# Kernel optimization log

Measured on AMD Instinct MI355X. Metric: run time of the kernel, lower is better.

The kernel has to match this reference:

```python
import jax, jax.numpy as jnp
import numpy as np

B, S, D = 8, 2048, 1024
N = 256          # state_dim
H = 512          # selector_hidden
E = 8            # num_experts


def murmurhash3_finalizer(token_ids):
    # Torch code works in int64 but masks to 32 bits after each multiply and
    # values stay non-negative, so it is exactly uint32 wrapping arithmetic.
    x = token_ids.astype(jnp.uint32)
    x = x ^ (x >> 16)
    x = x * jnp.uint32(2246822507)
    x = x ^ (x >> 13)
    x = x * jnp.uint32(3266489909)
    x = x ^ (x >> 16)
    return x


def setup_inputs() -> dict:
    key = jax.random.key(0)
    ks = jax.random.split(key, 7)
    scale = 0.02
    return {
        "x": jax.random.normal(ks[0], (B, S, D), dtype=jnp.float32),
        "token_ids": jax.random.randint(ks[1], (B, S), 0, 50257, dtype=jnp.int32),
        "Win": jax.random.normal(ks[2], (E, N, D), dtype=jnp.float32) * scale,      # in_proj.weight per expert
        "Wsin": jax.random.normal(ks[3], (E, H, D), dtype=jnp.float32) * scale,     # selector_in.weight
        "Wsout": jax.random.normal(ks[4], (E, 4 * N, H), dtype=jnp.float32) * scale,  # selector_out.weight
        "Wout": jax.random.normal(ks[5], (E, D, N), dtype=jnp.float32) * scale,     # out_proj.weight
        "dparam": jnp.ones((E, N), dtype=jnp.float32),                              # per-expert d
    }


def _forward(x, Win, Wsin, Wsout, Wout, dparam, token_ids):
    b, s, d = x.shape
    e_num, n, _ = Win.shape
    routes = (murmurhash3_finalizer(token_ids) % jnp.uint32(e_num)).astype(jnp.int32)  # (B,S)

    # Per-token expert projections, selected by hash route (masked accumulation
    # over the small fixed expert count; honors per-token routing).
    u = jnp.zeros((b, s, n), x.dtype)
    a = jnp.zeros((b, s, n), x.dtype)
    bg = jnp.zeros((b, s, n), x.dtype)
    c = jnp.zeros((b, s, n), x.dtype)
    dg = jnp.zeros((b, s, n), x.dtype)
    for e in range(e_num):
        m = (routes == e)[..., None]
        u = jnp.where(m, jnp.einsum('bsd,nd->bsn', x, Win[e]), u)
        sh = jax.nn.silu(jnp.einsum('bsd,hd->bsh', x, Wsin[e]))
        sel = jnp.einsum('bsh,oh->bso', sh, Wsout[e])       # (B,S,4N)
        ar, br, cr, dr = jnp.split(sel, 4, axis=-1)
        a = jnp.where(m, jax.nn.sigmoid(ar), a)
        bg = jnp.where(m, jnp.tanh(br), bg)
        c = jnp.where(m, jnp.tanh(cr), c)
        dg = jnp.where(m, jax.nn.sigmoid(dr), dg)

    dvec = dparam[routes]              # (B,S,N) expert d param per token
    skip = dvec * dg * u               # residual term, state-independent

    bidx = jnp.arange(b)

    def step(states, inp):
        # states: (B,E,N) per-expert hidden state per batch row
        route_t, u_t, a_t, b_t, c_t, skip_t = inp
        h_prev = states[bidx, route_t]                 # (B,N)
        h = a_t * h_prev + b_t * u_t
        states = states.at[bidx, route_t].set(h)       # only routed expert updates
        y = c_t * h + skip_t
        return states, y

    xs = (routes.swapaxes(0, 1), u.swapaxes(0, 1), a.swapaxes(0, 1),
          bg.swapaxes(0, 1), c.swapaxes(0, 1), skip.swapaxes(0, 1))
    states0 = jnp.zeros((b, e_num, n), x.dtype)
    _, ys = jax.lax.scan(step, states0, xs)            # ys: (S,B,N)
    y = ys.swapaxes(0, 1)                              # (B,S,N)

    out = jnp.zeros((b, s, d), x.dtype)
    for e in range(e_num):
        m = (routes == e)[..., None]
        out = jnp.where(m, jnp.einsum('bsn,dn->bsd', y, Wout[e]), out)
    return out


def reference(x, token_ids, Win, Wsin, Wsout, Wout, dparam):
    return _forward(x, Win, Wsin, Wsout, Wout, dparam, token_ids)
```

## Files before the change

kernel.cpp:

```cpp
#include <hip/hip_runtime.h>


#define TOKS 16384
#define RPAD 16512
#define DD   1024
#define NN   256
#define HH   512
#define MAXTILES  136
#define MAXCHUNKS 1088
#define CHUNK 16

typedef short short8 __attribute__((ext_vector_type(8)));
typedef float floatx4 __attribute__((ext_vector_type(4)));
typedef _Float16 half_t;

#define AS_GLOBAL __attribute__((address_space(1)))
#define AS_LDS    __attribute__((address_space(3)))

__device__ __forceinline__ void gl_lds16(const void* g, void* l) {
    __builtin_amdgcn_global_load_lds((const AS_GLOBAL void*)g, (AS_LDS void*)l, 16, 0, 0);
}

__device__ __forceinline__ unsigned short f2bf(float f) {
    union { float f; unsigned u; } c; c.f = f;
    unsigned r = c.u + 0x7FFF + ((c.u >> 16) & 1);
    return (unsigned short)(r >> 16);
}
__device__ __forceinline__ int route_of(int token) {
    unsigned x = (unsigned)token;
    x ^= x >> 16; x *= 2246822507u; x ^= x >> 13; x *= 3266489909u; x ^= x >> 16;
    return (int)(x & 7u);
}
__device__ __forceinline__ float sigm(float v) { return 1.0f / (1.0f + __expf(-v)); }
__device__ __forceinline__ float ftanh(float v) {
    float e = __expf(2.0f * v);
    return 1.0f - 2.0f / (e + 1.0f);
}

__global__ void k_route(const int* __restrict__ tok, int* __restrict__ cnt) {
    int b = blockIdx.x, tid = threadIdx.x;
    __shared__ int lc[256 * 8];
    #pragma unroll
    for (int e = 0; e < 8; e++) lc[tid * 8 + e] = 0;
    #pragma unroll
    for (int i = 0; i < 8; i++) {
        int e = route_of(tok[b * 2048 + tid * 8 + i]);
        lc[tid * 8 + e]++;
    }
    __syncthreads();
    if (tid < 8) {
        int s = 0;
        for (int t = 0; t < 256; t++) s += lc[t * 8 + tid];
        cnt[b * 8 + tid] = s;
    }
}

__global__ void k_offsets(const int* __restrict__ cnt, int* __restrict__ grpoff,
                          int* __restrict__ tileE, int* __restrict__ tileS,
                          int* __restrict__ tileR,
                          int* __restrict__ cGrp, int* __restrict__ cStart,
                          int* __restrict__ cLen, int* __restrict__ gBase,
                          int* __restrict__ meta) {
    __shared__ int sc[64], ce[8], eoff[9], etile[9], gb[65], go[64];
    int tid = threadIdx.x;
    if (tid < 64) sc[tid] = cnt[tid];
    __syncthreads();
    if (tid < 8) { int s = 0; for (int b = 0; b < 8; b++) s += sc[b * 8 + tid]; ce[tid] = s; }
    __syncthreads();
    if (tid == 0) {
        eoff[0] = 0; etile[0] = 0;
        for (int e = 0; e < 8; e++) {
            eoff[e + 1] = eoff[e] + ce[e];
            etile[e + 1] = etile[e] + (ce[e] + 127) / 128;
        }
        meta[0] = etile[8];
        gb[0] = 0;
        for (int g = 0; g < 64; g++) gb[g + 1] = gb[g] + (sc[g] + CHUNK - 1) / CHUNK;
        meta[1] = gb[64];
    }
    __syncthreads();
    if (tid < 64) {
        int b = tid >> 3, e = tid & 7;
        int run = eoff[e];
        for (int b2 = 0; b2 < b; b2++) run += sc[b2 * 8 + e];
        go[tid] = run;
        grpoff[tid] = run;
    }
    __syncthreads();
    if (tid < 8) {
        int e = tid, st = eoff[e], c = ce[e], t0 = etile[e];
        for (int i = 0, k = 0; i < c; i += 128, k++) {
            tileE[t0 + k] = e; tileS[t0 + k] = st + i;
            tileR[t0 + k] = (c - i < 128) ? (c - i) : 128;
        }
    }
    if (tid < 64) {
        int g = tid, n = sc[g], base = gb[g], s0 = go[g];
        gBase[g] = base;
        for (int i = 0, c = 0; i < n; i += CHUNK, c++) {
            cGrp[base + c] = g;
            cStart[base + c] = s0 + i;
            cLen[base + c] = (n - i < CHUNK) ? (n - i) : CHUNK;
        }
    }
}

__global__ void k_scatter(const int* __restrict__ tok, const int* __restrict__ grpoff,
                          int* __restrict__ perm) {
    int b = blockIdx.x, tid = threadIdx.x;
    __shared__ int lh[8 * 256];
    int r[8];
    int myc[8] = {0,0,0,0,0,0,0,0};
    #pragma unroll
    for (int i = 0; i < 8; i++) {
        int e = route_of(tok[b * 2048 + tid * 8 + i]);
        r[i] = e; myc[e]++;
    }
    #pragma unroll
    for (int e = 0; e < 8; e++) lh[e * 256 + tid] = myc[e];
    __syncthreads();
    for (int e = 0; e < 8; e++) {
        for (int off = 1; off < 256; off <<= 1) {
            int add = (tid >= off) ? lh[e * 256 + tid - off] : 0;
            __syncthreads();
            lh[e * 256 + tid] += add;
            __syncthreads();
        }
    }
    int basep[8];
    #pragma unroll
    for (int e = 0; e < 8; e++) basep[e] = grpoff[b * 8 + e] + lh[e * 256 + tid] - myc[e];
    #pragma unroll
    for (int i = 0; i < 8; i++) {
        int e = r[i];
        perm[basep[e]++] = b * 2048 + tid * 8 + i;
    }
}

__global__ void k_cvtw(const float* __restrict__ Win, const float* __restrict__ Wsin,
                       const float* __restrict__ Wsout, const float* __restrict__ Wout,
                       unsigned short* __restrict__ W12, unsigned short* __restrict__ Wso,
                       unsigned short* __restrict__ Wo) {
    const int C12 = 8 * 768 * 1024 / 4, CSO = 8 * 1024 * 512 / 4, CWO = 8 * 1024 * 256 / 4;
    int c = blockIdx.x * 256 + threadIdx.x;
    float4 v; unsigned short* dst;
    if (c < C12) {
        int d = c * 4;
        int e = d / (768 * 1024);
        int rem = d - e * (768 * 1024);
        int r = rem >> 10, k = rem & 1023;
        const float* src = (r < 256) ? (Win + (((size_t)e * 256 + r) << 10) + k)
                                     : (Wsin + (((size_t)e * 512 + (r - 256)) << 10) + k);
        v = *(const float4*)src;
        dst = W12 + d;
    } else if (c < C12 + CSO) {
        int d = (c - C12) * 4;
        v = *(const float4*)(Wsout + d);
        dst = Wso + d;
    } else if (c < C12 + CSO + CWO) {
        int d = (c - C12 - CSO) * 4;
        v = *(const float4*)(Wout + d);
        dst = Wo + d;
    } else return;
    ushort4 o;
    o.x = f2bf(v.x); o.y = f2bf(v.y); o.z = f2bf(v.z); o.w = f2bf(v.w);
    *(ushort4*)dst = o;
}

__global__ void k_gather(const float* __restrict__ x, const int* __restrict__ perm,
                         unsigned short* __restrict__ Xs, unsigned short* __restrict__ SHb,
                         unsigned short* __restrict__ Yb) {
    int r = blockIdx.x, t = threadIdx.x;
    if (r < TOKS) {
        int tok = perm[r];
        float4 v = *(const float4*)(x + (size_t)tok * 1024 + t * 4);
        ushort4 o;
        o.x = f2bf(v.x); o.y = f2bf(v.y); o.z = f2bf(v.z); o.w = f2bf(v.w);
        *(ushort4*)(Xs + (size_t)r * 1024 + t * 4) = o;
    } else {
        ushort4 z = {0, 0, 0, 0};
        *(ushort4*)(Xs + (size_t)r * 1024 + t * 4) = z;
        if (t < 128) *(ushort4*)(SHb + (size_t)r * 512 + t * 4) = z;
        if (t < 64)  *(ushort4*)(Yb + (size_t)r * 256 + t * 4) = z;
    }
}

template<int MODE, int KD>
__global__ __launch_bounds__(256, 3)
void k_mfma(const unsigned short* __restrict__ A, const unsigned short* __restrict__ Bw,
            const int* __restrict__ perm, const float* __restrict__ dparam,
            half_t* __restrict__ Ub, unsigned short* __restrict__ SHb,
            half_t* __restrict__ Aa, half_t* __restrict__ Wg,
            half_t* __restrict__ Cc, half_t* __restrict__ Sk,
            float* __restrict__ out,
            const int* __restrict__ tileE, const int* __restrict__ tileS,
            const int* __restrict__ tileR, const int* __restrict__ meta) {
    int mt = blockIdx.x;
    if (mt >= meta[0]) return;
    const int e = tileE[mt], pos0 = tileS[mt], rows = tileR[mt];
    const int col0 = blockIdx.y * 128;
    const int tid = threadIdx.x;
    const int w = tid >> 6, lane = tid & 63, quad = lane >> 4, l15 = lane & 15;
    const int wm = w & 1, wn = w >> 1;
    constexpr int NOUT = (MODE == 0) ? 768 : 1024;

    __shared__ unsigned short As[2 * 128 * 32];
    __shared__ unsigned short Bs[2 * 128 * 32];

    const int r0 = tid >> 2, c8 = (tid & 3) * 8;
    const unsigned short* ga = A + (size_t)(pos0 + r0) * KD + c8;
    const unsigned short* gb = Bw + ((size_t)e * NOUT + col0 + r0) * KD + c8;

    floatx4 acc[4][4] = {};

    int aoff[4], boff[4];
    #pragma unroll
    for (int i = 0; i < 4; i++) aoff[i] = (wm * 64 + i * 16 + l15) * 32 + quad * 8;
    #pragma unroll
    for (int j = 0; j < 4; j++) boff[j] = (wn * 64 + j * 16 + l15) * 32 + quad * 8;

    for (int k0 = 0; k0 < KD; k0 += 64) {
        __syncthreads();
        gl_lds16(ga + k0,                          As + w * 512);
        gl_lds16(ga + (size_t)64 * KD + k0,        As + 2048 + w * 512);
        gl_lds16(ga + k0 + 32,                     As + 4096 + w * 512);
        gl_lds16(ga + (size_t)64 * KD + k0 + 32,   As + 6144 + w * 512);
        gl_lds16(gb + k0,                          Bs + w * 512);
        gl_lds16(gb + (size_t)64 * KD + k0,        Bs + 2048 + w * 512);
        gl_lds16(gb + k0 + 32,                     Bs + 4096 + w * 512);
        gl_lds16(gb + (size_t)64 * KD + k0 + 32,   Bs + 6144 + w * 512);
        __syncthreads();
        #pragma unroll
        for (int kb = 0; kb < 2; kb++) {
            short8 af[4], bf[4];
            #pragma unroll
            for (int i = 0; i < 4; i++) af[i] = *(const short8*)(As + kb * 4096 + aoff[i]);
            #pragma unroll
            for (int j = 0; j < 4; j++) bf[j] = *(const short8*)(Bs + kb * 4096 + boff[j]);
            #pragma unroll
            for (int i = 0; i < 4; i++)
                #pragma unroll
                for (int j = 0; j < 4; j++)
                    acc[i][j] = __builtin_amdgcn_mfma_f32_16x16x32_bf16(af[i], bf[j], acc[i][j], 0, 0, 0);
        }
    }

    #pragma unroll
    for (int i = 0; i < 4; i++) {
        #pragma unroll
        for (int r = 0; r < 4; r++) {
            int m = wm * 64 + i * 16 + quad * 4 + r;
            if (m >= rows) continue;
            size_t row = (size_t)(pos0 + m);
            if (MODE == 0) {
                if (col0 < 256) {
                    #pragma unroll
                    for (int j = 0; j < 4; j++) {
                        int n = col0 + wn * 64 + j * 16 + l15;
                        Ub[row * 256 + n] = (half_t)acc[i][j][r];
                    }
                } else {
                    #pragma unroll
                    for (int j = 0; j < 4; j++) {
                        int n = col0 - 256 + wn * 64 + j * 16 + l15;
                        float v = acc[i][j][r];
                        SHb[row * 512 + n] = f2bf(v * sigm(v));
                    }
                }
            } else if (MODE == 1) {
                int region = col0 >> 8;
                #pragma unroll
                for (int j = 0; j < 4; j++) {
                    int n0 = (col0 & 255) + wn * 64 + j * 16 + l15;
                    size_t idx = row * 256 + (size_t)n0;
                    float v = acc[i][j][r];
                    if (region == 0) {
                        Aa[idx] = (half_t)sigm(v);
                    } else if (region == 1) {
                        Wg[idx] = (half_t)(ftanh(v) * (float)Ub[idx]);
                    } else if (region == 2) {
                        Cc[idx] = (half_t)ftanh(v);
                    } else {
                        Sk[idx] = (half_t)(dparam[e * 256 + n0] * sigm(v) * (float)Ub[idx]);
                    }
                }
            } else {
                int tok = perm[row];
                #pragma unroll
                for (int j = 0; j < 4; j++) {
                    int n = col0 + wn * 64 + j * 16 + l15;
                    out[(size_t)tok * 1024 + n] = acc[i][j][r];
                }
            }
        }
    }
}

__global__ void k_scanA(const half_t* __restrict__ Aa, const half_t* __restrict__ Wg,
                        const int* __restrict__ cStart, const int* __restrict__ cLen,
                        const int* __restrict__ meta,
                        float* __restrict__ SA, float* __restrict__ SQ) {
    int id = blockIdx.x;
    if (id >= meta[1]) return;
    int t = threadIdx.x;
    int s0 = cStart[id], L = cLen[id];
    size_t idx = (size_t)s0 * 256 + t;
    float p = 1.0f, q = 0.0f;
    for (int i = 0; i < L; i++) {
        float a = (float)Aa[idx], ww = (float)Wg[idx];
        q = a * q + ww;
        p *= a;
        idx += 256;
    }
    SA[(size_t)id * 256 + t] = p;
    SQ[(size_t)id * 256 + t] = q;
}

__global__ void k_scanB(const float* __restrict__ SA, const float* __restrict__ SQ,
                        const int* __restrict__ gBase, const int* __restrict__ cnt,
                        float* __restrict__ Hin) {
    int g = blockIdx.x, t = threadIdx.x;
    int base = gBase[g], nch = (cnt[g] + CHUNK - 1) / CHUNK;
    float h = 0.0f;
    for (int c = 0; c < nch; c++) {
        size_t k = (size_t)(base + c) * 256 + t;
        Hin[k] = h;
        h = SA[k] * h + SQ[k];
    }
}

__global__ void k_scanC(const half_t* __restrict__ Aa, const half_t* __restrict__ Wg,
                        const half_t* __restrict__ Cc, const half_t* __restrict__ Sk,
                        const int* __restrict__ cStart, const int* __restrict__ cLen,
                        const int* __restrict__ meta, const float* __restrict__ Hin,
                        unsigned short* __restrict__ Yb) {
    int id = blockIdx.x;
    if (id >= meta[1]) return;
    int t = threadIdx.x;
    int s0 = cStart[id], L = cLen[id];
    float h = Hin[(size_t)id * 256 + t];
    size_t idx = (size_t)s0 * 256 + t;
    for (int i = 0; i < L; i++) {
        float a = (float)Aa[idx], ww = (float)Wg[idx];
        float c = (float)Cc[idx], sk = (float)Sk[idx];
        h = a * h + ww;
        Yb[idx] = f2bf(c * h + sk);
        idx += 256;
    }
}

extern "C" void kernel_launch(void* const* d_in, const int* in_sizes, int n_in,
                              void* d_out, int out_size, void* d_ws, size_t ws_size,
                              hipStream_t stream) {
    const float* xin   = (const float*)d_in[0];
    const int*   tok   = (const int*)d_in[1];
    const float* Win   = (const float*)d_in[2];
    const float* Wsin  = (const float*)d_in[3];
    const float* Wsout = (const float*)d_in[4];
    const float* Wout  = (const float*)d_in[5];
    const float* dpar  = (const float*)d_in[6];
    float* out = (float*)d_out;

    size_t off = 0;
    char* base = (char*)d_ws;
    auto alloc = [&](size_t bytes) -> void* {
        void* p = base + off;
        off += (bytes + 255) & ~(size_t)255;
        return p;
    };
    half_t*         Ub  = (half_t*)alloc((size_t)RPAD * NN * 2);
    unsigned short* SHb = (unsigned short*)alloc((size_t)RPAD * HH * 2);
    unsigned short* Xs  = (unsigned short*)alloc((size_t)RPAD * DD * 2);
    unsigned short* Yb  = (unsigned short*)alloc((size_t)RPAD * NN * 2);
    half_t* Aa = (half_t*)alloc((size_t)TOKS * NN * 2);
    half_t* Wg = (half_t*)alloc((size_t)TOKS * NN * 2);
    half_t* Cc = (half_t*)alloc((size_t)TOKS * NN * 2);
    half_t* Sk = (half_t*)alloc((size_t)TOKS * NN * 2);
    unsigned short* W12 = (unsigned short*)alloc((size_t)8 * 768 * 1024 * 2);
    unsigned short* Wso = (unsigned short*)alloc((size_t)8 * 1024 * 512 * 2);
    unsigned short* Wo  = (unsigned short*)alloc((size_t)8 * 1024 * 256 * 2);
    float* SA  = (float*)alloc((size_t)MAXCHUNKS * 256 * 4);
    float* SQ  = (float*)alloc((size_t)MAXCHUNKS * 256 * 4);
    float* Hin = (float*)alloc((size_t)MAXCHUNKS * 256 * 4);
    int* perm   = (int*)alloc(TOKS * 4);
    int* cnt    = (int*)alloc(64 * 4);
    int* grpoff = (int*)alloc(64 * 4);
    int* tileE  = (int*)alloc(MAXTILES * 4);
    int* tileS  = (int*)alloc(MAXTILES * 4);
    int* tileR  = (int*)alloc(MAXTILES * 4);
    int* cGrp   = (int*)alloc(MAXCHUNKS * 4);
    int* cStart = (int*)alloc(MAXCHUNKS * 4);
    int* cLen   = (int*)alloc(MAXCHUNKS * 4);
    int* gBase  = (int*)alloc(64 * 4);
    int* meta   = (int*)alloc(16 * 4);

    k_route<<<8, 256, 0, stream>>>(tok, cnt);
    k_offsets<<<1, 256, 0, stream>>>(cnt, grpoff, tileE, tileS, tileR,
                                     cGrp, cStart, cLen, gBase, meta);
    k_scatter<<<8, 256, 0, stream>>>(tok, grpoff, perm);
    k_cvtw<<<12288, 256, 0, stream>>>(Win, Wsin, Wsout, Wout, W12, Wso, Wo);
    k_gather<<<RPAD, 256, 0, stream>>>(xin, perm, Xs, SHb, Yb);

    k_mfma<0, 1024><<<dim3(MAXTILES, 6), 256, 0, stream>>>(Xs, W12, perm, dpar,
        Ub, SHb, Aa, Wg, Cc, Sk, out, tileE, tileS, tileR, meta);
    k_mfma<1, 512><<<dim3(MAXTILES, 8), 256, 0, stream>>>(SHb, Wso, perm, dpar,
        Ub, SHb, Aa, Wg, Cc, Sk, out, tileE, tileS, tileR, meta);

    k_scanA<<<MAXCHUNKS, 256, 0, stream>>>(Aa, Wg, cStart, cLen, meta, SA, SQ);
    k_scanB<<<64, 256, 0, stream>>>(SA, SQ, gBase, cnt, Hin);
    k_scanC<<<MAXCHUNKS, 256, 0, stream>>>(Aa, Wg, Cc, Sk, cStart, cLen, meta, Hin, Yb);

    k_mfma<2, 256><<<dim3(MAXTILES, 8), 256, 0, stream>>>(Yb, Wo, perm, dpar,
        Ub, SHb, Aa, Wg, Cc, Sk, out, tileE, tileS, tileR, meta);
}
```

Before: 350.0 us.

## Double-buffer LDS tiles with async prefetch and XOR-swizzle to avoid bank conflicts

The MFMA GEMM main loop now ping-pongs between two LDS buffers of K=32 each, issuing global-to-LDS loads for the next slice before computing the current one, and uses explicit vmcnt waits and barriers. This overlaps memory latency with MFMA work instead of serializing load, sync and compute. It also XOR-swizzles the 8-element column chunk in both the store and the fragment read addresses to reduce LDS bank conflicts. In exchange each step covers half the previous K depth, so there are more barriers per tile, and correctness now depends on the hand-placed waitcnt counts.

```diff
diff --git a/kernel.cpp b/kernel.cpp
--- a/kernel.cpp
+++ b/kernel.cpp
@@ -203,47 +203,60 @@
     const int w = tid >> 6, lane = tid & 63, quad = lane >> 4, l15 = lane & 15;
     const int wm = w & 1, wn = w >> 1;
     constexpr int NOUT = (MODE == 0) ? 768 : 1024;
-
-    __shared__ unsigned short As[2 * 128 * 32];
-    __shared__ unsigned short Bs[2 * 128 * 32];
-
-    const int r0 = tid >> 2, c8 = (tid & 3) * 8;
-    const unsigned short* ga = A + (size_t)(pos0 + r0) * KD + c8;
-    const unsigned short* gb = Bw + ((size_t)e * NOUT + col0 + r0) * KD + c8;
+    constexpr int NK = KD / 32;
+
+    __shared__ unsigned short As[2][128 * 32];
+    __shared__ unsigned short Bs[2][128 * 32];
+
+    const int r0 = tid >> 2;
+    const int c8s = ((tid & 3) ^ ((tid >> 3) & 3)) * 8;
+    const unsigned short* ga = A + (size_t)(pos0 + r0) * KD + c8s;
+    const unsigned short* gb = Bw + ((size_t)e * NOUT + col0 + r0) * KD + c8s;
 
     floatx4 acc[4][4] = {};
 
+    const int sq = (quad ^ ((l15 >> 1) & 3)) * 8;
     int aoff[4], boff[4];
     #pragma unroll
-    for (int i = 0; i < 4; i++) aoff[i] = (wm * 64 + i * 16 + l15) * 32 + quad * 8;
-    #pragma unroll
-    for (int j = 0; j < 4; j++) boff[j] = (wn * 64 + j * 16 + l15) * 32 + quad * 8;
-
-    for (int k0 = 0; k0 < KD; k0 += 64) {
-        __syncthreads();
-        gl_lds16(ga + k0,                          As + w * 512);
-        gl_lds16(ga + (size_t)64 * KD + k0,        As + 2048 + w * 512);
-        gl_lds16(ga + k0 + 32,                     As + 4096 + w * 512);
-        gl_lds16(ga + (size_t)64 * KD + k0 + 32,   As + 6144 + w * 512);
-        gl_lds16(gb + k0,                          Bs + w * 512);
-        gl_lds16(gb + (size_t)64 * KD + k0,        Bs + 2048 + w * 512);
-        gl_lds16(gb + k0 + 32,                     Bs + 4096 + w * 512);
-        gl_lds16(gb + (size_t)64 * KD + k0 + 32,   Bs + 6144 + w * 512);
-        __syncthreads();
+    for (int i = 0; i < 4; i++) aoff[i] = (wm * 64 + i * 16 + l15) * 32 + sq;
+    #pragma unroll
+    for (int j = 0; j < 4; j++) boff[j] = (wn * 64 + j * 16 + l15) * 32 + sq;
+
+    #define STAGE(buf, k0) do { \
+        gl_lds16(ga + (k0),                    As[buf] + w * 512); \
+        gl_lds16(ga + (size_t)64 * KD + (k0),  As[buf] + 2048 + w * 512); \
+        gl_lds16(gb + (k0),                    Bs[buf] + w * 512); \
+        gl_lds16(gb + (size_t)64 * KD + (k0),  Bs[buf] + 2048 + w * 512); \
+    } while (0)
+
+    STAGE(0, 0);
+    for (int kt = 0; kt < NK; kt++) {
+        const int cur = kt & 1;
+        if (kt + 1 < NK) {
+            STAGE(cur ^ 1, (kt + 1) * 32);
+            asm volatile("s_waitcnt vmcnt(4)" ::: "memory");
+        } else {
+            asm volatile("s_waitcnt vmcnt(0)" ::: "memory");
+        }
+        __builtin_amdgcn_s_barrier();
+        asm volatile("" ::: "memory");
+        short8 af[4], bf[4];
         #pragma unroll
-        for (int kb = 0; kb < 2; kb++) {
-            short8 af[4], bf[4];
+        for (int i = 0; i < 4; i++) af[i] = *(const short8*)(As[cur] + aoff[i]);
+        #pragma unroll
+        for (int j = 0; j < 4; j++) bf[j] = *(const short8*)(Bs[cur] + boff[j]);
+        #pragma unroll
+        for (int i = 0; i < 4; i++)
             #pragma unroll
-            for (int i = 0; i < 4; i++) af[i] = *(const short8*)(As + kb * 4096 + aoff[i]);
-            #pragma unroll
-            for (int j = 0; j < 4; j++) bf[j] = *(const short8*)(Bs + kb * 4096 + boff[j]);
-            #pragma unroll
-            for (int i = 0; i < 4; i++)
-                #pragma unroll
-                for (int j = 0; j < 4; j++)
-                    acc[i][j] = __builtin_amdgcn_mfma_f32_16x16x32_bf16(af[i], bf[j], acc[i][j], 0, 0, 0);
-        }
-    }
+            for (int j = 0; j < 4; j++)
+                acc[i][j] = __builtin_amdgcn_mfma_f32_16x16x32_bf16(af[i], bf[j], acc[i][j], 0, 0, 0);
+        if (kt + 1 < NK) {
+            asm volatile("s_waitcnt lgkmcnt(0)" ::: "memory");
+            __builtin_amdgcn_s_barrier();
+        }
+    }
+    #undef STAGE
+    asm volatile("" ::: "memory");
 
     #pragma unroll
     for (int i = 0; i < 4; i++) {
```

Measured after the change: 348.9 us. About the same (-0.3%).
